# Performance work log

Hardware: AMD Instinct MI355X
Metric: run time of the kernel (lower is better)

## Reference

```python
import jax, jax.numpy as jnp
from jax import lax
import numpy as np

B, T = 1024, 1024
IN_F, H1, H2 = 1, 64, 32  # n_features, hidden_dim, emb_dim


def setup_inputs() -> dict:
    key = jax.random.key(0)
    ks = jax.random.split(key, 9)
    s1 = 1.0 / np.sqrt(H1)
    s2 = 1.0 / np.sqrt(H2)
    u = lambda k, shape, s: jax.random.uniform(k, shape, jnp.float32, -s, s)
    return {
        "x": jax.random.normal(ks[0], (B, T), jnp.float32),
        "W_ih1": u(ks[1], (3 * H1, IN_F), s1),
        "W_hh1": u(ks[2], (3 * H1, H1), s1),
        "b_ih1": u(ks[3], (3 * H1,), s1),
        "b_hh1": u(ks[4], (3 * H1,), s1),
        "W_ih2": u(ks[5], (3 * H2, H1), s2),
        "W_hh2": u(ks[6], (3 * H2, H2), s2),
        "b_ih2": u(ks[7], (3 * H2,), s2),
        "b_hh2": u(ks[8], (3 * H2,), s2),
    }


def _gru(x_tm, W_ih, b_ih, W_hh, b_hh):
    """PyTorch-convention GRU over time-major input x_tm [T, B, F].
    Returns (all hidden states [T, B, H], final hidden [B, H])."""
    Tn, Bn, _ = x_tm.shape
    H = W_hh.shape[1]
    # Precompute input projections for all timesteps: [T, B, 3H]
    gx = jnp.einsum('tbf,gf->tbg', x_tm, W_ih) + b_ih

    def step(h, gx_t):
        gh = h @ W_hh.T + b_hh  # [B, 3H]
        r = jax.nn.sigmoid(gx_t[:, :H] + gh[:, :H])
        z = jax.nn.sigmoid(gx_t[:, H:2 * H] + gh[:, H:2 * H])
        n = jnp.tanh(gx_t[:, 2 * H:] + r * gh[:, 2 * H:])
        h_new = (1.0 - z) * n + z * h
        return h_new, h_new

    h0 = jnp.zeros((Bn, H), x_tm.dtype)
    hT, ys = lax.scan(step, h0, gx)
    return ys, hT


def reference(x, W_ih1, W_hh1, b_ih1, b_hh1, W_ih2, W_hh2, b_ih2, b_hh2):
    x_tm = x.T[:, :, None]  # [T, B, 1] time-major
    out1, _ = _gru(x_tm, W_ih1, b_ih1, W_hh1, b_hh1)   # [T, B, H1]
    _, h2 = _gru(out1, W_ih2, b_ih2, W_hh2, b_hh2)      # [B, H2]
    return h2  # hidden[0] of rnn2: final hidden state [B, emb_dim]
```

## Files before the change

kernel.cpp:

```cpp
#include <hip/hip_runtime.h>

#define TSTEPS 1024
#define CH 4

typedef _Float16 half8  __attribute__((ext_vector_type(8)));
typedef float    f32x4  __attribute__((ext_vector_type(4)));

#define MFMA16(A_, B_, C_) __builtin_amdgcn_mfma_f32_16x16x32_f16((A_), (B_), (C_), 0, 0, 0)

__device__ __forceinline__ float fast_rcp(float x) { return __builtin_amdgcn_rcpf(x); }
__device__ __forceinline__ float fast_exp2(float x) {
#if __has_builtin(__builtin_amdgcn_exp2f)
    return __builtin_amdgcn_exp2f(x);
#else
    return exp2f(x);
#endif
}

__device__ __forceinline__ half8 load_w8s(const float* p, float s) {
    const float4 a = ((const float4*)p)[0];
    const float4 b = ((const float4*)p)[1];
    half8 r;
    r[0] = (_Float16)(s * a.x); r[1] = (_Float16)(s * a.y);
    r[2] = (_Float16)(s * a.z); r[3] = (_Float16)(s * a.w);
    r[4] = (_Float16)(s * b.x); r[5] = (_Float16)(s * b.y);
    r[6] = (_Float16)(s * b.z); r[7] = (_Float16)(s * b.w);
    return r;
}

__global__ __launch_bounds__(384, 1)
void gru2_encoder(const float* __restrict__ x,
                  const float* __restrict__ W_ih1,
                  const float* __restrict__ W_hh1,
                  const float* __restrict__ b_ih1,
                  const float* __restrict__ b_hh1,
                  const float* __restrict__ W_ih2,
                  const float* __restrict__ W_hh2,
                  const float* __restrict__ b_ih2,
                  const float* __restrict__ b_hh2,
                  float* __restrict__ out)
{
    const int blk  = blockIdx.x;
    const int tid  = threadIdx.x;
    const int lane = tid & 63;
    const int wid  = tid >> 6;
    const int nl   = lane & 15;
    const int quad = lane >> 4;
    const int ac   = nl >> 2;
    const int chain0 = blk * CH;

    const float SNEG = -1.44269504f;
    const float SP2  =  2.88539008f;

    __shared__ __align__(16) _Float16 s_h1[2][4][80];
    __shared__ __align__(16) _Float16 s_h2[2][4][48];
    __shared__ __align__(16) _Float16 s_x[TSTEPS][4];

    for (int idx = tid; idx < 4 * TSTEPS; idx += 384) {
        const int m = idx >> 10, t = idx & (TSTEPS - 1);
        s_x[t][m] = (_Float16)x[(size_t)(chain0 + m) * TSTEPS + t];
    }
    {
        _Float16* p1 = &s_h1[0][0][0];
        for (int idx = tid; idx < 2 * 4 * 80; idx += 384) p1[idx] = (_Float16)0.0f;
        _Float16* p2 = &s_h2[0][0][0];
        for (int idx = tid; idx < 2 * 4 * 48; idx += 384) p2[idx] = (_Float16)0.0f;
    }
    __syncthreads();

    if (wid < 4) {
        const int un = wid * 16 + nl;
        const half8 Br0 = load_w8s(W_hh1 + (size_t)(un)        * 64 + quad * 8,      SNEG);
        const half8 Br1 = load_w8s(W_hh1 + (size_t)(un)        * 64 + 32 + quad * 8, SNEG);
        const half8 Bz0 = load_w8s(W_hh1 + (size_t)(64 + un)   * 64 + quad * 8,      SNEG);
        const half8 Bz1 = load_w8s(W_hh1 + (size_t)(64 + un)   * 64 + 32 + quad * 8, SNEG);
        const half8 Bn0 = load_w8s(W_hh1 + (size_t)(128 + un)  * 64 + quad * 8,      SP2);
        const half8 Bn1 = load_w8s(W_hh1 + (size_t)(128 + un)  * 64 + 32 + quad * 8, SP2);
        const float cr = SNEG * (b_ih1[un] + b_hh1[un]);
        const float cz = SNEG * (b_ih1[64 + un] + b_hh1[64 + un]);
        const float cn = SP2 * b_hh1[128 + un];
        const f32x4 Cr = {cr, cr, cr, cr};
        const f32x4 Cz = {cz, cz, cz, cz};
        const f32x4 Cn = {cn, cn, cn, cn};
        const float twr = SNEG * W_ih1[un];
        const float twz = SNEG * W_ih1[64 + un];
        const float twn = SP2  * W_ih1[128 + un];
        const float tbn = SP2  * b_ih1[128 + un];

        float h1s = 0.0f;

        for (int t = 0; t <= TSTEPS; ++t) {
            if (t < TSTEPS) {
                const int pr = (t + 1) & 1;
                const half8 A0 = *(const half8*)&s_h1[pr][ac][quad * 8];
                const half8 A1 = *(const half8*)&s_h1[pr][ac][32 + quad * 8];
                f32x4 aR = MFMA16(A0, Br0, Cr); aR = MFMA16(A1, Br1, aR);
                f32x4 aZ = MFMA16(A0, Bz0, Cz); aZ = MFMA16(A1, Bz1, aZ);
                f32x4 aN = MFMA16(A0, Bn0, Cn); aN = MFMA16(A1, Bn1, aN);
                const float xv = (float)s_x[t][quad];
                const float ea = fast_exp2(fmaf(twr, xv, aR[0]));
                const float eb = fast_exp2(fmaf(twz, xv, aZ[0]));
                const float d1 = 1.0f + ea, d2 = 1.0f + eb;
                const float inv = fast_rcp(d1 * d2);
                const float rg = d2 * inv, zg = d1 * inv;
                const float nx = fmaf(twn, xv, tbn);
                const float ec = fast_exp2(fmaf(rg, aN[0], nx));
                const float nn = fmaf(-2.0f, fast_rcp(ec + 1.0f), 1.0f);
                h1s = nn + zg * (h1s - nn);
                s_h1[t & 1][quad][un] = (_Float16)h1s;
            }
            __syncthreads();
        }
    } else {
        const int vn = (wid - 4) * 16 + nl;
        const half8 BiR0 = load_w8s(W_ih2 + (size_t)(vn)      * 64 + quad * 8,      SNEG);
        const half8 BiR1 = load_w8s(W_ih2 + (size_t)(vn)      * 64 + 32 + quad * 8, SNEG);
        const half8 BiZ0 = load_w8s(W_ih2 + (size_t)(32 + vn) * 64 + quad * 8,      SNEG);
        const half8 BiZ1 = load_w8s(W_ih2 + (size_t)(32 + vn) * 64 + 32 + quad * 8, SNEG);
        const half8 BiN0 = load_w8s(W_ih2 + (size_t)(64 + vn) * 64 + quad * 8,      SP2);
        const half8 BiN1 = load_w8s(W_ih2 + (size_t)(64 + vn) * 64 + 32 + quad * 8, SP2);
        const half8 BhR  = load_w8s(W_hh2 + (size_t)(vn)      * 32 + quad * 8,      SNEG);
        const half8 BhZ  = load_w8s(W_hh2 + (size_t)(32 + vn) * 32 + quad * 8,      SNEG);
        const half8 BhN  = load_w8s(W_hh2 + (size_t)(64 + vn) * 32 + quad * 8,      SP2);
        const float gr  = SNEG * (b_ih2[vn] + b_hh2[vn]);
        const float gz  = SNEG * (b_ih2[32 + vn] + b_hh2[32 + vn]);
        const float gnx = SP2 * b_ih2[64 + vn];
        const float gnh = SP2 * b_hh2[64 + vn];
        const f32x4 Gr  = {gr, gr, gr, gr};
        const f32x4 Gz  = {gz, gz, gz, gz};
        const f32x4 Gnx = {gnx, gnx, gnx, gnx};
        const f32x4 Gnh = {gnh, gnh, gnh, gnh};

        float h2s = 0.0f;

        for (int t = 0; t <= TSTEPS; ++t) {
            if (t >= 1) {
                const int pA = (t + 1) & 1;
                const half8 A0 = *(const half8*)&s_h1[pA][ac][quad * 8];
                const half8 A1 = *(const half8*)&s_h1[pA][ac][32 + quad * 8];
                const half8 Ah = *(const half8*)&s_h2[t & 1][ac][quad * 8];
                f32x4 aR = MFMA16(A0, BiR0, Gr);  aR = MFMA16(A1, BiR1, aR);
                aR = MFMA16(Ah, BhR, aR);
                f32x4 aZ = MFMA16(A0, BiZ0, Gz);  aZ = MFMA16(A1, BiZ1, aZ);
                aZ = MFMA16(Ah, BhZ, aZ);
                f32x4 aNx = MFMA16(A0, BiN0, Gnx); aNx = MFMA16(A1, BiN1, aNx);
                f32x4 aNh = MFMA16(Ah, BhN, Gnh);
                const float ea = fast_exp2(aR[0]);
                const float eb = fast_exp2(aZ[0]);
                const float d1 = 1.0f + ea, d2 = 1.0f + eb;
                const float inv = fast_rcp(d1 * d2);
                const float rg = d2 * inv, zg = d1 * inv;
                const float ec = fast_exp2(fmaf(rg, aNh[0], aNx[0]));
                const float n2 = fmaf(-2.0f, fast_rcp(ec + 1.0f), 1.0f);
                h2s = n2 + zg * (h2s - n2);
                s_h2[(t + 1) & 1][quad][vn] = (_Float16)h2s;
            }
            __syncthreads();
        }

        out[(size_t)(chain0 + quad) * 32 + vn] = h2s;
    }
}

extern "C" void kernel_launch(void* const* d_in, const int* in_sizes, int n_in,
                              void* d_out, int out_size, void* d_ws, size_t ws_size,
                              hipStream_t stream) {
    const float* x     = (const float*)d_in[0];
    const float* W_ih1 = (const float*)d_in[1];
    const float* W_hh1 = (const float*)d_in[2];
    const float* b_ih1 = (const float*)d_in[3];
    const float* b_hh1 = (const float*)d_in[4];
    const float* W_ih2 = (const float*)d_in[5];
    const float* W_hh2 = (const float*)d_in[6];
    const float* b_ih2 = (const float*)d_in[7];
    const float* b_hh2 = (const float*)d_in[8];
    float* out = (float*)d_out;

    gru2_encoder<<<dim3(1024 / CH), dim3(384), 0, stream>>>(
        x, W_ih1, W_hh1, b_ih1, b_hh1, W_ih2, W_hh2, b_ih2, b_hh2, out);
}
```

Measured before the change: 311.4 us.

## Pack two chain sets per block with 768 threads and halve grid

Each block now processes two independent groups of 4 batch chains (8 chains) using 12 waves: 8 for layer 1 and 4 for layer 2. Shared hidden-state and input buffers gain a set dimension, and the grid is halved to 128 blocks. The intent is to give each CU more independent work so the latency of the serial recurrence is better hidden. The trade-off is that only half the CUs are used, each SIMD carries more MFMA and transcendental work per step, and each block-wide barrier now spans 12 waves.

Measured after the change: 401.9 us. +29.0%, slower.

```diff
diff --git a/kernel.cpp b/kernel.cpp
--- a/kernel.cpp
+++ b/kernel.cpp
@@ -2,6 +2,7 @@
 
 #define TSTEPS 1024
 #define CH 4
+#define SETS 2
 
 typedef _Float16 half8  __attribute__((ext_vector_type(8)));
 typedef float    f32x4  __attribute__((ext_vector_type(4)));
@@ -28,7 +29,7 @@
     return r;
 }
 
-__global__ __launch_bounds__(384, 1)
+__global__ __launch_bounds__(768, 1)
 void gru2_encoder(const float* __restrict__ x,
                   const float* __restrict__ W_ih1,
                   const float* __restrict__ W_hh1,
@@ -47,29 +48,31 @@
     const int nl   = lane & 15;
     const int quad = lane >> 4;
     const int ac   = nl >> 2;
-    const int chain0 = blk * CH;
+    const int chain0 = blk * (CH * SETS);
 
     const float SNEG = -1.44269504f;
     const float SP2  =  2.88539008f;
 
-    __shared__ __align__(16) _Float16 s_h1[2][4][80];
-    __shared__ __align__(16) _Float16 s_h2[2][4][48];
-    __shared__ __align__(16) _Float16 s_x[TSTEPS][4];
+    __shared__ __align__(16) _Float16 s_h1[2][SETS][4][80];
+    __shared__ __align__(16) _Float16 s_h2[2][SETS][4][48];
+    __shared__ __align__(16) _Float16 s_x[TSTEPS][8];
 
-    for (int idx = tid; idx < 4 * TSTEPS; idx += 384) {
+    for (int idx = tid; idx < 8 * TSTEPS; idx += 768) {
         const int m = idx >> 10, t = idx & (TSTEPS - 1);
         s_x[t][m] = (_Float16)x[(size_t)(chain0 + m) * TSTEPS + t];
     }
     {
-        _Float16* p1 = &s_h1[0][0][0];
-        for (int idx = tid; idx < 2 * 4 * 80; idx += 384) p1[idx] = (_Float16)0.0f;
-        _Float16* p2 = &s_h2[0][0][0];
-        for (int idx = tid; idx < 2 * 4 * 48; idx += 384) p2[idx] = (_Float16)0.0f;
+        _Float16* p1 = &s_h1[0][0][0][0];
+        for (int idx = tid; idx < 2 * SETS * 4 * 80; idx += 768) p1[idx] = (_Float16)0.0f;
+        _Float16* p2 = &s_h2[0][0][0][0];
+        for (int idx = tid; idx < 2 * SETS * 4 * 48; idx += 768) p2[idx] = (_Float16)0.0f;
     }
     __syncthreads();
 
-    if (wid < 4) {
-        const int un = wid * 16 + nl;
+    if (wid < 8) {
+        const int st  = wid >> 2;
+        const int g1t = wid & 3;
+        const int un  = g1t * 16 + nl;
         const half8 Br0 = load_w8s(W_hh1 + (size_t)(un)        * 64 + quad * 8,      SNEG);
         const half8 Br1 = load_w8s(W_hh1 + (size_t)(un)        * 64 + 32 + quad * 8, SNEG);
         const half8 Bz0 = load_w8s(W_hh1 + (size_t)(64 + un)   * 64 + quad * 8,      SNEG);
@@ -92,12 +95,12 @@
         for (int t = 0; t <= TSTEPS; ++t) {
             if (t < TSTEPS) {
                 const int pr = (t + 1) & 1;
-                const half8 A0 = *(const half8*)&s_h1[pr][ac][quad * 8];
-                const half8 A1 = *(const half8*)&s_h1[pr][ac][32 + quad * 8];
+                const half8 A0 = *(const half8*)&s_h1[pr][st][ac][quad * 8];
+                const half8 A1 = *(const half8*)&s_h1[pr][st][ac][32 + quad * 8];
                 f32x4 aR = MFMA16(A0, Br0, Cr); aR = MFMA16(A1, Br1, aR);
                 f32x4 aZ = MFMA16(A0, Bz0, Cz); aZ = MFMA16(A1, Bz1, aZ);
                 f32x4 aN = MFMA16(A0, Bn0, Cn); aN = MFMA16(A1, Bn1, aN);
-                const float xv = (float)s_x[t][quad];
+                const float xv = (float)s_x[t][st * 4 + quad];
                 const float ea = fast_exp2(fmaf(twr, xv, aR[0]));
                 const float eb = fast_exp2(fmaf(twz, xv, aZ[0]));
                 const float d1 = 1.0f + ea, d2 = 1.0f + eb;
@@ -107,12 +110,14 @@
                 const float ec = fast_exp2(fmaf(rg, aN[0], nx));
                 const float nn = fmaf(-2.0f, fast_rcp(ec + 1.0f), 1.0f);
                 h1s = nn + zg * (h1s - nn);
-                s_h1[t & 1][quad][un] = (_Float16)h1s;
+                s_h1[t & 1][st][quad][un] = (_Float16)h1s;
             }
             __syncthreads();
         }
     } else {
-        const int vn = (wid - 4) * 16 + nl;
+        const int st  = (wid - 8) >> 1;
+        const int g2t = (wid - 8) & 1;
+        const int vn  = g2t * 16 + nl;
         const half8 BiR0 = load_w8s(W_ih2 + (size_t)(vn)      * 64 + quad * 8,      SNEG);
         const half8 BiR1 = load_w8s(W_ih2 + (size_t)(vn)      * 64 + 32 + quad * 8, SNEG);
         const half8 BiZ0 = load_w8s(W_ih2 + (size_t)(32 + vn) * 64 + quad * 8,      SNEG);
@@ -136,9 +141,9 @@
         for (int t = 0; t <= TSTEPS; ++t) {
             if (t >= 1) {
                 const int pA = (t + 1) & 1;
-                const half8 A0 = *(const half8*)&s_h1[pA][ac][quad * 8];
-                const half8 A1 = *(const half8*)&s_h1[pA][ac][32 + quad * 8];
-                const half8 Ah = *(const half8*)&s_h2[t & 1][ac][quad * 8];
+                const half8 A0 = *(const half8*)&s_h1[pA][st][ac][quad * 8];
+                const half8 A1 = *(const half8*)&s_h1[pA][st][ac][32 + quad * 8];
+                const half8 Ah = *(const half8*)&s_h2[t & 1][st][ac][quad * 8];
                 f32x4 aR = MFMA16(A0, BiR0, Gr);  aR = MFMA16(A1, BiR1, aR);
                 aR = MFMA16(Ah, BhR, aR);
                 f32x4 aZ = MFMA16(A0, BiZ0, Gz);  aZ = MFMA16(A1, BiZ1, aZ);
@@ -153,12 +158,12 @@
                 const float ec = fast_exp2(fmaf(rg, aNh[0], aNx[0]));
                 const float n2 = fmaf(-2.0f, fast_rcp(ec + 1.0f), 1.0f);
                 h2s = n2 + zg * (h2s - n2);
-                s_h2[(t + 1) & 1][quad][vn] = (_Float16)h2s;
+                s_h2[(t + 1) & 1][st][quad][vn] = (_Float16)h2s;
             }
             __syncthreads();
         }
 
-        out[(size_t)(chain0 + quad) * 32 + vn] = h2s;
+        out[(size_t)(chain0 + st * 4 + quad) * 32 + vn] = h2s;
     }
 }
 
@@ -176,6 +181,6 @@
     const float* b_hh2 = (const float*)d_in[8];
     float* out = (float*)d_out;
 
-    gru2_encoder<<<dim3(1024 / CH), dim3(384), 0, stream>>>(
+    gru2_encoder<<<dim3(1024 / (CH * SETS)), dim3(768), 0, stream>>>(
         x, W_ih1, W_hh1, b_ih1, b_hh1, W_ih2, W_hh2, b_ih2, b_hh2, out);
 }
```
